# Kernel tuning notes

Hardware: AMD Instinct MI355X
Metric: run time of the kernel (lower is better)

Reference implementation:

```python
import jax, jax.numpy as jnp
import numpy as np

EPSILON = 1.5  # quality-tolerance threshold from init_kwargs
NEG_INF = -1000000000.0


def setup_inputs() -> dict:
    key = jax.random.key(0)
    k1, k2, k3 = jax.random.split(key, 3)
    B, S, D, E = 4, 4096, 2048, 64
    return {
        "hidden_states": jax.random.normal(k1, (B, S, D), dtype=jnp.float32),
        "gate_W": jax.random.normal(k2, (E, D), dtype=jnp.float32),  # nn.Linear weight [out,in]
        "secret_projection": jax.random.normal(k3, (D, E), dtype=jnp.float32),
        "top_k": 2,
    }


def reference(hidden_states, gate_W, secret_projection, top_k):
    # raw gate logits: Linear without bias -> x @ W^T
    raw_logits = jnp.einsum("bsd,ed->bse", hidden_states, gate_W)
    # watermark bias via secret LSH projection
    watermark_bias = jnp.einsum("bsd,de->bse", hidden_states, secret_projection)
    # indifference zone: experts whose logit is within epsilon of the max
    max_logits = jnp.max(raw_logits, axis=-1, keepdims=True)
    safe_mask = raw_logits >= max_logits - EPSILON
    modified_scores = jnp.where(safe_mask, watermark_bias, jnp.asarray(NEG_INF, raw_logits.dtype))
    # top-k over watermark-preferred safe experts
    _, selected_experts = jax.lax.top_k(modified_scores, top_k)
    # gather original logits at selected experts, softmax over the k slots
    router_logits = jnp.take_along_axis(raw_logits, selected_experts, axis=-1)
    routing_weights = jax.nn.softmax(router_logits, axis=-1)
    return routing_weights, selected_experts
```

## Files before the change

### kernel.cpp

```cpp
#include <hip/hip_runtime.h>
#include <stdint.h>


#define DDIM 2048
#define NEXP 64
#define NT   64
#define NEG_INF  -1000000000.0f
#define MRG_RAW  0.04f
#define MRG_WM   0.15f

typedef __attribute__((ext_vector_type(8))) short bf16x8;
typedef __attribute__((ext_vector_type(4))) float f32x4;

union BFrag { bf16x8 v; uint32_t w[4]; uint4 q; };

__device__ inline void split8_rne(const float* a, bf16x8* hi, bf16x8* lo) {
    BFrag h, l;
    #pragma unroll
    for (int p = 0; p < 4; ++p) {
        const uint32_t u0 = __float_as_uint(a[2*p]);
        const uint32_t u1 = __float_as_uint(a[2*p+1]);
        const uint32_t h0 = (u0 + 0x7FFFu + ((u0 >> 16) & 1u)) >> 16;
        const uint32_t h1 = (u1 + 0x7FFFu + ((u1 >> 16) & 1u)) >> 16;
        const float r0 = a[2*p]   - __uint_as_float(h0 << 16);
        const float r1 = a[2*p+1] - __uint_as_float(h1 << 16);
        const uint32_t v0 = __float_as_uint(r0);
        const uint32_t v1 = __float_as_uint(r1);
        const uint32_t l0 = (v0 + 0x7FFFu + ((v0 >> 16) & 1u)) >> 16;
        const uint32_t l1 = (v1 + 0x7FFFu + ((v1 >> 16) & 1u)) >> 16;
        h.w[p] = h0 | (h1 << 16);
        l.w[p] = l0 | (l1 << 16);
    }
    *hi = h.v; *lo = l.v;
}

__device__ inline void split8t(const float* a, bf16x8* hi, bf16x8* lo) {
    BFrag h, l;
    #pragma unroll
    for (int p = 0; p < 4; ++p) {
        const uint32_t u0 = __float_as_uint(a[2*p]);
        const uint32_t u1 = __float_as_uint(a[2*p+1]);
        h.w[p] = (u0 >> 16) | (u1 & 0xFFFF0000u);
        const float r0 = a[2*p]   - __uint_as_float(u0 & 0xFFFF0000u);
        const float r1 = a[2*p+1] - __uint_as_float(u1 & 0xFFFF0000u);
        l.w[p] = (__float_as_uint(r0) >> 16) | (__float_as_uint(r1) & 0xFFFF0000u);
    }
    *hi = h.v; *lo = l.v;
}

__global__ void prep_b(const float* __restrict__ gateW, const float* __restrict__ secret,
                       uint4* __restrict__ wsB) {
    const int kstep = blockIdx.x;
    const int s = threadIdx.x >> 6;
    const int l = threadIdx.x & 63;
    const int col = s * 16 + (l & 15);
    const int kb  = kstep * 32 + (l >> 4) * 8;
    float v[8];
    if (col < NEXP) {
        #pragma unroll
        for (int j = 0; j < 8; ++j) v[j] = gateW[(size_t)col * DDIM + kb + j];
    } else {
        #pragma unroll
        for (int j = 0; j < 8; ++j) v[j] = secret[(size_t)(kb + j) * NEXP + (col - NEXP)];
    }
    bf16x8 hi, lo; split8_rne(v, &hi, &lo);
    const size_t base = (size_t)(kstep * 8 + s) * 128 + l;
    BFrag t;
    t.v = hi; wsB[base]      = t.q;
    t.v = lo; wsB[base + 64] = t.q;
}

__device__ inline void gl_lds16(const char* g, char* l) {
    __builtin_amdgcn_global_load_lds(
        (const __attribute__((address_space(1))) void*)g,
        (__attribute__((address_space(3))) void*)l, 16, 0, 0);
}

__global__ __launch_bounds__(256, 1)
void gemm_lds(const float* __restrict__ x, const char* __restrict__ wsB,
              float* __restrict__ wsL, int ntok)
{
    __shared__ __align__(16) char lds[2][16384];

    const int tid = threadIdx.x;
    const int w = tid >> 6, l = tid & 63;
    const int c = l & 15;
    const int g = l >> 4;
    const int rowbase = blockIdx.x * 64 + w * 16;

    f32x4 acc[8];
    #pragma unroll
    for (int s = 0; s < 8; ++s) acc[s] = (f32x4){0.f, 0.f, 0.f, 0.f};

    const float* xr = x + (size_t)(rowbase + c) * DDIM + g * 8;

    #define STAGE(ts, buf)                                                        \
        {                                                                         \
            _Pragma("unroll")                                                     \
            for (int j = 0; j < 4; ++j) {                                         \
                const int f = j * 4 + w;                                          \
                const int s_ = f >> 1, hl = f & 1;                                \
                gl_lds16(wsB + ((size_t)((ts) * 8 + s_) * 128 + hl * 64 + l) * 16,\
                         &lds[buf][f * 1024 + l * 16]);                           \
            }                                                                     \
        }

    float4 A0a, A0b, A1a, A1b;
    STAGE(0, 0);
    A0a = *reinterpret_cast<const float4*>(xr);
    A0b = *reinterpret_cast<const float4*>(xr + 4);

    for (int ts = 0; ts < NT; ++ts) {
        __syncthreads();

        if (ts < NT - 1) {
            STAGE(ts + 1, (ts + 1) & 1);
            A1a = *reinterpret_cast<const float4*>(xr + (ts + 1) * 32);
            A1b = *reinterpret_cast<const float4*>(xr + (ts + 1) * 32 + 4);
        }

        const float va[8] = {A0a.x, A0a.y, A0a.z, A0a.w, A0b.x, A0b.y, A0b.z, A0b.w};
        bf16x8 ah, al;
        split8t(va, &ah, &al);

        const char* bb = lds[ts & 1];
        #pragma unroll
        for (int s = 0; s < 8; ++s) {
            const bf16x8 bh = *reinterpret_cast<const bf16x8*>(bb + (2*s)     * 1024 + l * 16);
            const bf16x8 bl = *reinterpret_cast<const bf16x8*>(bb + (2*s + 1) * 1024 + l * 16);
            acc[s] = __builtin_amdgcn_mfma_f32_16x16x32_bf16(ah, bh, acc[s], 0, 0, 0);
            acc[s] = __builtin_amdgcn_mfma_f32_16x16x32_bf16(ah, bl, acc[s], 0, 0, 0);
            acc[s] = __builtin_amdgcn_mfma_f32_16x16x32_bf16(al, bh, acc[s], 0, 0, 0);
        }
        A0a = A1a; A0b = A1b;
    }
    #undef STAGE

    #pragma unroll
    for (int s = 0; s < 8; ++s)
        #pragma unroll
        for (int r = 0; r < 4; ++r)
            wsL[(size_t)(rowbase + g * 4 + r) * 128 + s * 16 + c] = acc[s][r];
}

__global__ __launch_bounds__(256, 4)
void router_k(const float* __restrict__ wsL,
              const float* __restrict__ x,
              const float* __restrict__ gateW,
              const float* __restrict__ secret,
              float* __restrict__ out, int ntok)
{
    const int t = blockIdx.x * 4 + (threadIdx.x >> 6);
    const int e = threadIdx.x & 63;

    float raw = wsL[(size_t)t * 128 + e];
    float wm  = wsL[(size_t)t * 128 + NEXP + e];

    float rmax = raw;
    #pragma unroll
    for (int off = 32; off; off >>= 1) rmax = fmaxf(rmax, __shfl_xor(rmax, off));

    if (__any(fabsf(raw - (rmax - 1.5f)) < MRG_RAW)) {
        float s0 = 0.f, s1 = 0.f, s2 = 0.f, s3 = 0.f;
        const float4* xr = reinterpret_cast<const float4*>(x + (size_t)t * DDIM);
        const float4* wr = reinterpret_cast<const float4*>(gateW + (size_t)e * DDIM);
        for (int k = 0; k < DDIM / 4; ++k) {
            const float4 a = xr[k], b = wr[k];
            s0 = fmaf(a.x, b.x, s0); s1 = fmaf(a.y, b.y, s1);
            s2 = fmaf(a.z, b.z, s2); s3 = fmaf(a.w, b.w, s3);
        }
        raw = (s0 + s1) + (s2 + s3);
        rmax = raw;
        #pragma unroll
        for (int off = 32; off; off >>= 1) rmax = fmaxf(rmax, __shfl_xor(rmax, off));
    }

    const bool safe = (raw >= rmax - 1.5f);
    float m = safe ? wm : NEG_INF;

    float v1 = m; int e1 = e;
    #pragma unroll
    for (int off = 32; off; off >>= 1) {
        const float ov = __shfl_xor(v1, off); const int oi = __shfl_xor(e1, off);
        if (ov > v1 || (ov == v1 && oi < e1)) { v1 = ov; e1 = oi; }
    }
    float v2 = (e == e1) ? -3.0e38f : m; int e2 = e;
    #pragma unroll
    for (int off = 32; off; off >>= 1) {
        const float ov = __shfl_xor(v2, off); const int oi = __shfl_xor(e2, off);
        if (ov > v2 || (ov == v2 && oi < e2)) { v2 = ov; e2 = oi; }
    }
    float v3 = (e == e1 || e == e2) ? -3.0e38f : m; int e3 = e;
    #pragma unroll
    for (int off = 32; off; off >>= 1) {
        const float ov = __shfl_xor(v3, off); const int oi = __shfl_xor(e3, off);
        if (ov > v3 || (ov == v3 && oi < e3)) { v3 = ov; e3 = oi; }
    }

    const bool wmRisk = (v2 > NEG_INF + 1.0f && v1 - v2 < MRG_WM) ||
                        (v3 > NEG_INF + 1.0f && v2 - v3 < MRG_WM);
    if (__any(wmRisk)) {
        float s0 = 0.f, s1 = 0.f, s2 = 0.f, s3 = 0.f;
        const float* xr = x + (size_t)t * DDIM;
        for (int k = 0; k < DDIM; k += 4) {
            s0 = fmaf(xr[k + 0], secret[(size_t)(k + 0) * NEXP + e], s0);
            s1 = fmaf(xr[k + 1], secret[(size_t)(k + 1) * NEXP + e], s1);
            s2 = fmaf(xr[k + 2], secret[(size_t)(k + 2) * NEXP + e], s2);
            s3 = fmaf(xr[k + 3], secret[(size_t)(k + 3) * NEXP + e], s3);
        }
        m = safe ? ((s0 + s1) + (s2 + s3)) : NEG_INF;
        v1 = m; e1 = e;
        #pragma unroll
        for (int off = 32; off; off >>= 1) {
            const float ov = __shfl_xor(v1, off); const int oi = __shfl_xor(e1, off);
            if (ov > v1 || (ov == v1 && oi < e1)) { v1 = ov; e1 = oi; }
        }
        v2 = (e == e1) ? -3.0e38f : m; e2 = e;
        #pragma unroll
        for (int off = 32; off; off >>= 1) {
            const float ov = __shfl_xor(v2, off); const int oi = __shfl_xor(e2, off);
            if (ov > v2 || (ov == v2 && oi < e2)) { v2 = ov; e2 = oi; }
        }
    }

    const float l1 = __shfl(raw, e1);
    const float l2 = __shfl(raw, e2);

    if (e == 0) {
        const float mm = fmaxf(l1, l2);
        const float x1 = expf(l1 - mm), x2 = expf(l2 - mm);
        const float inv = 1.0f / (x1 + x2);
        out[(size_t)t * 2 + 0] = x1 * inv;
        out[(size_t)t * 2 + 1] = x2 * inv;
        out[(size_t)2 * ntok + t * 2 + 0] = (float)e1;
        out[(size_t)2 * ntok + t * 2 + 1] = (float)e2;
    }
}

extern "C" void kernel_launch(void* const* d_in, const int* in_sizes, int n_in,
                              void* d_out, int out_size, void* d_ws, size_t ws_size,
                              hipStream_t stream) {
    const float* x      = (const float*)d_in[0];
    const float* gateW  = (const float*)d_in[1];
    const float* secret = (const float*)d_in[2];
    float* out = (float*)d_out;

    const int ntok = in_sizes[0] / DDIM;
    uint4* wsB = (uint4*)d_ws;
    float* wsL = (float*)((char*)d_ws + (2u << 20));

    prep_b<<<64, 512, 0, stream>>>(gateW, secret, wsB);
    gemm_lds<<<ntok / 64, 256, 0, stream>>>(x, (const char*)wsB, wsL, ntok);
    router_k<<<ntok / 4, 256, 0, stream>>>(wsL, x, gateW, secret, out, ntok);
}
```

Before: 111.1 us.

## Split GEMM K dimension across wave pairs and halve rows per block

Each block now covers 32 token rows instead of 64. Its four waves split into two row groups and two K halves (split-K), and the two K-half partial sums are combined through LDS at the end. The grid doubles to 512 blocks and launch bounds allow two blocks per CU, to raise occupancy and spread work across the MI355X's CUs. In exchange, the B staging buffer per block doubles and an extra LDS reduction with two barriers is added.

After: 97.96 us. 11.8% less time.

```diff
diff --git a/kernel.cpp b/kernel.cpp
--- a/kernel.cpp
+++ b/kernel.cpp
@@ -4,10 +4,11 @@
 
 #define DDIM 2048
 #define NEXP 64
-#define NT   64
+#define NT   32
 #define NEG_INF  -1000000000.0f
 #define MRG_RAW  0.04f
 #define MRG_WM   0.15f
+#define RST      130
 
 typedef __attribute__((ext_vector_type(8))) short bf16x8;
 typedef __attribute__((ext_vector_type(4))) float f32x4;
@@ -76,33 +77,37 @@
         (__attribute__((address_space(3))) void*)l, 16, 0, 0);
 }
 
-__global__ __launch_bounds__(256, 1)
+__global__ __launch_bounds__(256, 2)
 void gemm_lds(const float* __restrict__ x, const char* __restrict__ wsB,
               float* __restrict__ wsL, int ntok)
 {
-    __shared__ __align__(16) char lds[2][16384];
+    __shared__ __align__(16) char lds[2][32768];
 
     const int tid = threadIdx.x;
     const int w = tid >> 6, l = tid & 63;
+    const int p = w & 1;
+    const int h = w >> 1;
     const int c = l & 15;
     const int g = l >> 4;
-    const int rowbase = blockIdx.x * 64 + w * 16;
+    const int rowbase = blockIdx.x * 32 + p * 16;
 
     f32x4 acc[8];
     #pragma unroll
     for (int s = 0; s < 8; ++s) acc[s] = (f32x4){0.f, 0.f, 0.f, 0.f};
 
-    const float* xr = x + (size_t)(rowbase + c) * DDIM + g * 8;
-
-    #define STAGE(ts, buf)                                                        \
-        {                                                                         \
-            _Pragma("unroll")                                                     \
-            for (int j = 0; j < 4; ++j) {                                         \
-                const int f = j * 4 + w;                                          \
-                const int s_ = f >> 1, hl = f & 1;                                \
-                gl_lds16(wsB + ((size_t)((ts) * 8 + s_) * 128 + hl * 64 + l) * 16,\
-                         &lds[buf][f * 1024 + l * 16]);                           \
-            }                                                                     \
+    const float* xr = x + (size_t)(rowbase + c) * DDIM + h * 1024 + g * 8;
+
+    #define STAGE(ts, buf)                                                          \
+        {                                                                           \
+            _Pragma("unroll")                                                       \
+            for (int j = 0; j < 8; ++j) {                                           \
+                const int F  = j * 4 + w;                                \
+                const int fs = ((F >> 4) << 5) + (ts);                              \
+                const int i  = F & 15;                                              \
+                gl_lds16(wsB + ((size_t)(fs * 8 + (i >> 1)) * 128                   \
+                                + (i & 1) * 64 + l) * 16,                           \
+                         &lds[buf][F * 1024 + l * 16]);                             \
+            }                                                                       \
         }
 
     float4 A0a, A0b, A1a, A1b;
@@ -123,7 +128,7 @@
         bf16x8 ah, al;
         split8t(va, &ah, &al);
 
-        const char* bb = lds[ts & 1];
+        const char* bb = lds[ts & 1] + h * 16384;
         #pragma unroll
         for (int s = 0; s < 8; ++s) {
             const bf16x8 bh = *reinterpret_cast<const bf16x8*>(bb + (2*s)     * 1024 + l * 16);
@@ -136,11 +141,27 @@
     }
     #undef STAGE
 
-    #pragma unroll
-    for (int s = 0; s < 8; ++s)
-        #pragma unroll
-        for (int r = 0; r < 4; ++r)
-            wsL[(size_t)(rowbase + g * 4 + r) * 128 + s * 16 + c] = acc[s][r];
+    float* red = reinterpret_cast<float*>(&lds[0][0]);
+    __syncthreads();
+    if (h == 1) {
+        float* L = red + p * 16 * RST;
+        #pragma unroll
+        for (int s = 0; s < 8; ++s)
+            #pragma unroll
+            for (int r = 0; r < 4; ++r)
+                L[(g * 4 + r) * RST + s * 16 + c] = acc[s][r];
+    }
+    __syncthreads();
+    if (h == 0) {
+        const float* L = red + p * 16 * RST;
+        #pragma unroll
+        for (int s = 0; s < 8; ++s)
+            #pragma unroll
+            for (int r = 0; r < 4; ++r) {
+                const float v = acc[s][r] + L[(g * 4 + r) * RST + s * 16 + c];
+                wsL[(size_t)(rowbase + g * 4 + r) * 128 + s * 16 + c] = v;
+            }
+    }
 }
 
 __global__ __launch_bounds__(256, 4)
@@ -250,6 +271,6 @@
     float* wsL = (float*)((char*)d_ws + (2u << 20));
 
     prep_b<<<64, 512, 0, stream>>>(gateW, secret, wsB);
-    gemm_lds<<<ntok / 64, 256, 0, stream>>>(x, (const char*)wsB, wsL, ntok);
+    gemm_lds<<<ntok / 32, 256, 0, stream>>>(x, (const char*)wsB, wsL, ntok);
     router_k<<<ntok / 4, 256, 0, stream>>>(wsL, x, gateW, secret, out, ntok);
 }
```

## Split GEMM along K into four partial-sum blocks reduced in router

Applied to the files above, without the earlier changes.

The single GEMM kernel (256 blocks of 64 tokens over full K) becomes a split-K kernel where each token tile is handled by four blocks covering a quarter of K each. Partial logits go to separate workspace slices and are summed in the router kernel. This raises block count to fill the GPU's CUs and allows more blocks per CU, and it replaces the loop-top syncthreads with explicit waitcnt plus barrier. The cost is four times the partial-logit writes and reads, plus a workspace-size dependency with a fallback path.

New measurement: 94.84 us. -14.6%, faster.

```diff
diff --git a/kernel.cpp b/kernel.cpp
--- a/kernel.cpp
+++ b/kernel.cpp
@@ -4,7 +4,6 @@
 
 #define DDIM 2048
 #define NEXP 64
-#define NT   64
 #define NEG_INF  -1000000000.0f
 #define MRG_RAW  0.04f
 #define MRG_WM   0.15f
@@ -76,45 +75,52 @@
         (__attribute__((address_space(3))) void*)l, 16, 0, 0);
 }
 
-__global__ __launch_bounds__(256, 1)
-void gemm_lds(const float* __restrict__ x, const char* __restrict__ wsB,
-              float* __restrict__ wsL, int ntok)
+template <int KSPLIT>
+__global__ __launch_bounds__(256, 4)
+void gemm_q(const float* __restrict__ x, const char* __restrict__ wsB,
+            float* __restrict__ wsP, int ntok)
 {
+    const int NTS = (DDIM / KSPLIT) / 32;
     __shared__ __align__(16) char lds[2][16384];
 
     const int tid = threadIdx.x;
     const int w = tid >> 6, l = tid & 63;
     const int c = l & 15;
     const int g = l >> 4;
-    const int rowbase = blockIdx.x * 64 + w * 16;
+    const int q  = blockIdx.x & (KSPLIT - 1);
+    const int mb = blockIdx.x / KSPLIT;
+    const int rowbase = mb * 64 + w * 16;
 
     f32x4 acc[8];
     #pragma unroll
     for (int s = 0; s < 8; ++s) acc[s] = (f32x4){0.f, 0.f, 0.f, 0.f};
 
-    const float* xr = x + (size_t)(rowbase + c) * DDIM + g * 8;
-
-    #define STAGE(ts, buf)                                                        \
-        {                                                                         \
-            _Pragma("unroll")                                                     \
-            for (int j = 0; j < 4; ++j) {                                         \
-                const int f = j * 4 + w;                                          \
-                const int s_ = f >> 1, hl = f & 1;                                \
-                gl_lds16(wsB + ((size_t)((ts) * 8 + s_) * 128 + hl * 64 + l) * 16,\
-                         &lds[buf][f * 1024 + l * 16]);                           \
-            }                                                                     \
+    const float* xr = x + (size_t)(rowbase + c) * DDIM + q * (DDIM / KSPLIT) + g * 8;
+    const char*  bq = wsB + (size_t)(q * NTS) * 16384;
+
+    #define STAGE(ts, buf)                                                       \
+        {                                                                        \
+            _Pragma("unroll")                                                    \
+            for (int j = 0; j < 4; ++j) {                                        \
+                const int i = j * 4 + w;                                         \
+                gl_lds16(bq + ((size_t)((ts) * 8 + (i >> 1)) * 128               \
+                               + (i & 1) * 64 + l) * 16,                         \
+                         &lds[buf][i * 1024 + l * 16]);                          \
+            }                                                                    \
         }
 
     float4 A0a, A0b, A1a, A1b;
     STAGE(0, 0);
     A0a = *reinterpret_cast<const float4*>(xr);
     A0b = *reinterpret_cast<const float4*>(xr + 4);
-
-    for (int ts = 0; ts < NT; ++ts) {
-        __syncthreads();
-
-        if (ts < NT - 1) {
-            STAGE(ts + 1, (ts + 1) & 1);
+    asm volatile("s_waitcnt vmcnt(0)" ::: "memory");
+    __builtin_amdgcn_s_barrier();
+
+    #pragma unroll 1
+    for (int ts = 0; ts < NTS; ++ts) {
+        const int cur = ts & 1;
+        if (ts + 1 < NTS) {
+            STAGE(ts + 1, cur ^ 1);
             A1a = *reinterpret_cast<const float4*>(xr + (ts + 1) * 32);
             A1b = *reinterpret_cast<const float4*>(xr + (ts + 1) * 32 + 4);
         }
@@ -123,7 +129,7 @@
         bf16x8 ah, al;
         split8t(va, &ah, &al);
 
-        const char* bb = lds[ts & 1];
+        const char* bb = lds[cur];
         #pragma unroll
         for (int s = 0; s < 8; ++s) {
             const bf16x8 bh = *reinterpret_cast<const bf16x8*>(bb + (2*s)     * 1024 + l * 16);
@@ -132,19 +138,24 @@
             acc[s] = __builtin_amdgcn_mfma_f32_16x16x32_bf16(ah, bl, acc[s], 0, 0, 0);
             acc[s] = __builtin_amdgcn_mfma_f32_16x16x32_bf16(al, bh, acc[s], 0, 0, 0);
         }
+
+        asm volatile("s_waitcnt vmcnt(0)" ::: "memory");
+        __builtin_amdgcn_s_barrier();
         A0a = A1a; A0b = A1b;
     }
     #undef STAGE
 
+    const size_t MN = (size_t)ntok * 128;
     #pragma unroll
     for (int s = 0; s < 8; ++s)
         #pragma unroll
         for (int r = 0; r < 4; ++r)
-            wsL[(size_t)(rowbase + g * 4 + r) * 128 + s * 16 + c] = acc[s][r];
-}
-
+            wsP[(size_t)q * MN + (size_t)(rowbase + g * 4 + r) * 128 + s * 16 + c] = acc[s][r];
+}
+
+template <int KSPLIT>
 __global__ __launch_bounds__(256, 4)
-void router_k(const float* __restrict__ wsL,
+void router_k(const float* __restrict__ wsP,
               const float* __restrict__ x,
               const float* __restrict__ gateW,
               const float* __restrict__ secret,
@@ -152,9 +163,14 @@
 {
     const int t = blockIdx.x * 4 + (threadIdx.x >> 6);
     const int e = threadIdx.x & 63;
-
-    float raw = wsL[(size_t)t * 128 + e];
-    float wm  = wsL[(size_t)t * 128 + NEXP + e];
+    const size_t MN = (size_t)ntok * 128;
+
+    float raw = 0.f, wm = 0.f;
+    #pragma unroll
+    for (int q = 0; q < KSPLIT; ++q) {
+        raw += wsP[(size_t)q * MN + (size_t)t * 128 + e];
+        wm  += wsP[(size_t)q * MN + (size_t)t * 128 + NEXP + e];
+    }
 
     float rmax = raw;
     #pragma unroll
@@ -247,9 +263,16 @@
 
     const int ntok = in_sizes[0] / DDIM;
     uint4* wsB = (uint4*)d_ws;
-    float* wsL = (float*)((char*)d_ws + (2u << 20));
+    float* wsP = (float*)((char*)d_ws + (2u << 20));
+    const size_t MN4 = (size_t)ntok * 128 * 4;
 
     prep_b<<<64, 512, 0, stream>>>(gateW, secret, wsB);
-    gemm_lds<<<ntok / 64, 256, 0, stream>>>(x, (const char*)wsB, wsL, ntok);
-    router_k<<<ntok / 4, 256, 0, stream>>>(wsL, x, gateW, secret, out, ntok);
-}
+
+    if (ws_size >= (2u << 20) + 4 * MN4) {
+        gemm_q<4><<<(ntok / 64) * 4, 256, 0, stream>>>(x, (const char*)wsB, wsP, ntok);
+        router_k<4><<<ntok / 4, 256, 0, stream>>>(wsP, x, gateW, secret, out, ntok);
+    } else {
+        gemm_q<1><<<(ntok / 64), 256, 0, stream>>>(x, (const char*)wsB, wsP, ntok);
+        router_k<1><<<ntok / 4, 256, 0, stream>>>(wsP, x, gateW, secret, out, ntok);
+    }
+}
```
